# Optimization experiments

Measured on AMD Instinct MI355X. Metric: run time of the kernel, lower is better.

The kernel has to match this reference:

```python
import jax, jax.numpy as jnp
import numpy as np

N, E, D, T, R, H = 100000, 500000, 128, 3, 4, 8
DK = D // H
MAXLEN = 240
L = 2


def _rte_table():
    # Replicates RelTemporalEncoding sinusoidal table (note original precedence:
    # div_term = 1 / ((10000 ** arange(0, 2d, 2)) / d / 2); large exponents overflow
    # to inf in fp32 -> div entries become 0, matching torch behaviour).
    pos = jnp.arange(MAXLEN, dtype=jnp.float32)[:, None]            # [240, 1]
    ar = jnp.arange(0.0, 2 * D, 2.0, dtype=jnp.float32)             # [D]
    div = 1.0 / (jnp.power(jnp.float32(10000.0), ar) / D / 2.0)
    ang = pos * div                                                  # [240, D]
    s = np.float32(1.0 / np.sqrt(D))
    tab = jnp.zeros((MAXLEN, 2 * D), jnp.float32)
    tab = tab.at[:, 0::2].set(jnp.sin(ang) * s)
    tab = tab.at[:, 1::2].set(jnp.cos(ang) * s)
    return tab


def _typed_linear(x, W, b, types):
    # per-row type-specific affine: small fixed loop over node types
    out = jnp.zeros((x.shape[0], W.shape[-1]), x.dtype)
    for t in range(W.shape[0]):
        m = (types == t)[:, None].astype(x.dtype)
        out = out + m * (x @ W[t] + b[t])
    return out


def _typed_mm(x, W, types):
    out = jnp.zeros((x.shape[0], W.shape[-1]), x.dtype)
    for t in range(W.shape[0]):
        out = out + (types == t)[:, None].astype(x.dtype) * (x @ W[t])
    return out


def _hgt_layer(x, node_type, src, tgt, edge_type, edge_time, rte_tab,
               Wk, bk, Wq, bq, Wv, bv, Wa, ba, rel_pri, rel_att, rel_msg,
               skip, rte_w, rte_b):
    st = node_type[src]
    tt = node_type[tgt]
    # node-level typed projections (Q uses raw target feats; K/V bias+feat part)
    Qn = _typed_linear(x, Wq, bq, node_type)
    Kn = _typed_linear(x, Wk, bk, node_type)
    Vn = _typed_linear(x, Wv, bv, node_type)
    # per-edge temporal encoding added to source features before K/V linears;
    # linearity lets us add its typed projection (no double bias)
    rte = rte_tab[edge_time] @ rte_w + rte_b                         # [E, D]
    q = Qn[tgt].reshape(-1, H, DK)
    k = (Kn[src] + _typed_mm(rte, Wk, st)).reshape(-1, H, DK)
    v = (Vn[src] + _typed_mm(rte, Wv, st)).reshape(-1, H, DK)
    k2 = jnp.zeros_like(k)
    v2 = jnp.zeros_like(v)
    for r in range(R):  # small fixed relation loop, masked per-edge
        m = (edge_type == r)[:, None, None].astype(x.dtype)
        k2 = k2 + m * jnp.einsum('ehk,hkl->ehl', k, rel_att[r])
        v2 = v2 + m * jnp.einsum('ehk,hkl->ehl', v, rel_msg[r])
    pri = rel_pri[tt, edge_type, st]                                 # [E, H]
    score = (q * k2).sum(-1) * pri / np.float32(np.sqrt(DK))         # [E, H]
    # scatter-softmax over edges grouped by target node
    mx = jax.ops.segment_max(score, tgt, num_segments=N)
    ex = jnp.exp(score - mx[tgt])
    den = jax.ops.segment_sum(ex, tgt, num_segments=N)
    att = ex / den[tgt]
    msg = (v2 * att[:, :, None]).reshape(-1, D)
    aggr = jax.ops.segment_sum(msg, tgt, num_segments=N)             # [N, D]
    h = jax.nn.gelu(aggr, approximate=False)
    trans = _typed_linear(h, Wa, ba, node_type)
    alpha = jax.nn.sigmoid(skip)[node_type][:, None]
    return alpha * trans + (1.0 - alpha) * x


def setup_inputs() -> dict:
    key = jax.random.key(0)
    ks = jax.random.split(key, 20)
    s = np.float32(1.0 / np.sqrt(D))
    return {
        'node_feature': jax.random.normal(ks[0], (N, D), jnp.float32),
        'node_type': jax.random.randint(ks[1], (N,), 0, T, jnp.int32),
        'edge_index': jax.random.randint(ks[2], (2, E), 0, N, jnp.int32),
        'edge_type': jax.random.randint(ks[3], (E,), 0, R, jnp.int32),
        'edge_time': jax.random.randint(ks[4], (E,), 0, MAXLEN, jnp.int32),
        'adapt_w': jax.random.normal(ks[5], (T, D, D), jnp.float32) * s,
        'adapt_b': jax.random.normal(ks[6], (T, D), jnp.float32) * 0.01,
        'Wk': jax.random.normal(ks[7], (L, T, D, D), jnp.float32) * s,
        'bk': jax.random.normal(ks[8], (L, T, D), jnp.float32) * 0.01,
        'Wq': jax.random.normal(ks[9], (L, T, D, D), jnp.float32) * s,
        'bq': jax.random.normal(ks[10], (L, T, D), jnp.float32) * 0.01,
        'Wv': jax.random.normal(ks[11], (L, T, D, D), jnp.float32) * s,
        'bv': jax.random.normal(ks[12], (L, T, D), jnp.float32) * 0.01,
        'Wa': jax.random.normal(ks[13], (L, T, D, D), jnp.float32) * s,
        'ba': jax.random.normal(ks[14], (L, T, D), jnp.float32) * 0.01,
        'rel_pri': jnp.ones((L, T, R, T, H), jnp.float32),
        'rel_att': jax.random.normal(ks[15], (L, R, H, DK, DK), jnp.float32) * np.float32(1.0 / np.sqrt(DK)),
        'rel_msg': jax.random.normal(ks[16], (L, R, H, DK, DK), jnp.float32) * np.float32(1.0 / np.sqrt(DK)),
        'skip': jnp.ones((L, T), jnp.float32),
        'rte_w': jax.random.normal(ks[17], (L, 2 * D, D), jnp.float32) * np.float32(1.0 / np.sqrt(2 * D)),
        'rte_b': jax.random.normal(ks[18], (L, D), jnp.float32) * 0.01,
    }


def reference(node_feature, node_type, edge_index, edge_type, edge_time,
              adapt_w, adapt_b, Wk, bk, Wq, bq, Wv, bv, Wa, ba,
              rel_pri, rel_att, rel_msg, skip, rte_w, rte_b):
    rte_tab = _rte_table()
    src, tgt = edge_index[0], edge_index[1]
    # GNN input adaptation: typed linear + tanh (dropout = 0 / eval mode)
    x = jnp.tanh(_typed_linear(node_feature, adapt_w, adapt_b, node_type))
    for l in range(L):
        x = _hgt_layer(x, node_type, src, tgt, edge_type, edge_time, rte_tab,
                       Wk[l], bk[l], Wq[l], bq[l], Wv[l], bv[l], Wa[l], ba[l],
                       rel_pri[l], rel_att[l], rel_msg[l], skip[l],
                       rte_w[l], rte_b[l])
    return x
```

## Files before the change

kernel.cpp:

```cpp
#include <hip/hip_runtime.h>
#include <math.h>

#define NN 100000
#define EE 500000

__global__ void rte_tab_kernel(float* __restrict__ tab) {
    int p = blockIdx.x;
    int j = threadIdx.x;
    int m = j >> 1;
    float pf = (float)pow(10000.0, (double)(2 * m));
    float dv = 1.0f / (pf / 128.0f / 2.0f);
    float ang = (float)p * dv;
    const float s = 0.08838834764831845f;
    float v = (j & 1) ? (cosf(ang) * s) : (sinf(ang) * s);
    tab[p * 256 + j] = v;
}

__global__ void rte_proj_kernel(const float* __restrict__ tab,
                                const float* __restrict__ rte_w,
                                const float* __restrict__ rte_b,
                                float* __restrict__ proj) {
    __shared__ float row[256];
    int p = blockIdx.x;
    int c = threadIdx.x;
    for (int i = threadIdx.x; i < 256; i += 128) row[i] = tab[p * 256 + i];
    __syncthreads();
    float acc = rte_b[c];
    #pragma unroll 8
    for (int q = 0; q < 256; ++q) acc += row[q] * rte_w[q * 128 + c];
    proj[p * 128 + c] = acc;
}

__global__ void ktv_kernel(const float* __restrict__ proj,
                           const float* __restrict__ Wk,
                           const float* __restrict__ Wv,
                           float* __restrict__ ktv) {
    __shared__ float row[128];
    int b = blockIdx.x;
    int t = b / 240, p = b % 240;
    int c = threadIdx.x;
    row[c] = proj[p * 128 + c];
    __syncthreads();
    const float* wk = Wk + t * 16384 + c;
    const float* wv = Wv + t * 16384 + c;
    float ak = 0.f, av = 0.f;
    #pragma unroll 8
    for (int q = 0; q < 128; ++q) {
        float rv = row[q];
        ak += rv * wk[q * 128];
        av += rv * wv[q * 128];
    }
    ktv[(size_t)b * 256 + c] = ak;
    ktv[(size_t)b * 256 + 128 + c] = av;
}

__global__ void hist_kernel(const int* __restrict__ tgt, int* __restrict__ cnt) {
    int e = blockIdx.x * blockDim.x + threadIdx.x;
    if (e < EE) atomicAdd(&cnt[tgt[e]], 1);
}

__global__ void scan_kernel(const int* __restrict__ cnt, int* __restrict__ row_start) {
    __shared__ int sdata[1024];
    __shared__ int s_running;
    if (threadIdx.x == 0) s_running = 0;
    __syncthreads();
    for (int base = 0; base < NN; base += 1024) {
        int i = base + (int)threadIdx.x;
        int v = (i < NN) ? cnt[i] : 0;
        sdata[threadIdx.x] = v;
        __syncthreads();
        int acc = v;
        for (int off = 1; off < 1024; off <<= 1) {
            int t = (threadIdx.x >= (unsigned)off) ? sdata[threadIdx.x - off] : 0;
            __syncthreads();
            acc += t;
            sdata[threadIdx.x] = acc;
            __syncthreads();
        }
        int run = s_running;
        if (i < NN) row_start[i] = run + acc - v;
        __syncthreads();
        if (threadIdx.x == 1023) s_running = run + sdata[1023];
        __syncthreads();
    }
    if (threadIdx.x == 0) row_start[NN] = s_running;
}

__global__ void scatter_meta_kernel(const int* __restrict__ esrc,
                                    const int* __restrict__ etgt,
                                    const int* __restrict__ etype,
                                    const int* __restrict__ etime,
                                    const int* __restrict__ node_type,
                                    const int* __restrict__ row_start,
                                    int* __restrict__ fill,
                                    int4* __restrict__ meta) {
    int e = blockIdx.x * blockDim.x + threadIdx.x;
    if (e < EE) {
        int tgt = etgt[e];
        int src = esrc[e];
        int r = etype[e];
        int tm = etime[e];
        int st = node_type[src];
        int tt = node_type[tgt];
        int tb = st * 240 + tm;
        int pos = row_start[tgt] + atomicAdd(&fill[tgt], 1);
        meta[pos] = make_int4(src, (tb << 6) | (tt << 4) | (st << 2) | r, tgt, 0);
    }
}

__global__ void node_hist_kernel(const int* __restrict__ nt, int* __restrict__ tcnt) {
    __shared__ int lc[3];
    if (threadIdx.x < 3) lc[threadIdx.x] = 0;
    __syncthreads();
    int i = blockIdx.x * blockDim.x + threadIdx.x;
    if (i < NN) atomicAdd(&lc[nt[i]], 1);
    __syncthreads();
    if (threadIdx.x < 3) atomicAdd(&tcnt[threadIdx.x], lc[threadIdx.x]);
}

__global__ void node_scatter_kernel(const int* __restrict__ nt,
                                    const int* __restrict__ tcnt,
                                    int* __restrict__ fill3,
                                    int* __restrict__ order) {
    __shared__ int lc[3], lbase[3], lfill[3];
    if (threadIdx.x < 3) { lc[threadIdx.x] = 0; lfill[threadIdx.x] = 0; }
    __syncthreads();
    int i = blockIdx.x * blockDim.x + threadIdx.x;
    int t = -1;
    if (i < NN) { t = nt[i]; atomicAdd(&lc[t], 1); }
    __syncthreads();
    if (threadIdx.x < 3) lbase[threadIdx.x] = atomicAdd(&fill3[threadIdx.x], lc[threadIdx.x]);
    __syncthreads();
    if (i < NN) {
        int rank = atomicAdd(&lfill[t], 1);
        int tb = (t == 0) ? 0 : ((t == 1) ? tcnt[0] : tcnt[0] + tcnt[1]);
        order[tb + lbase[t] + rank] = i;
    }
}

template <int MODE>
__global__ __launch_bounds__(256) void typed_lin_kernel(
    const float* __restrict__ in, const int* __restrict__ nt,
    const int* __restrict__ order,
    const float* __restrict__ W, const float* __restrict__ b,
    const float* __restrict__ skip, float* __restrict__ out) {
    __shared__ float xs[32][128];
    __shared__ int rows[32];
    __shared__ int sty[32];
    int nb = blockIdx.x * 32;
    if (threadIdx.x < 32) {
        int r = order[nb + threadIdx.x];
        rows[threadIdx.x] = r;
        sty[threadIdx.x] = nt[r];
    }
    __syncthreads();
    for (int i = threadIdx.x; i < 1024; i += 256) {
        int nl = i >> 5, e4 = i & 31;
        *(float4*)&xs[nl][e4 * 4] = *(const float4*)(in + (size_t)rows[nl] * 128 + e4 * 4);
    }
    __syncthreads();
    int col = threadIdx.x & 127;
    int ng  = (threadIdx.x >> 7) * 16;
    int t0 = sty[ng];
    bool uni = true;
    #pragma unroll
    for (int ii = 1; ii < 16; ++ii) uni &= (sty[ng + ii] == t0);
    if (uni) {
        const float* w = W + t0 * 16384 + col;
        float bv = b[t0 * 128 + col];
        float alpha = (MODE == 1) ? (1.f / (1.f + __expf(-skip[t0]))) : 0.f;
        float acc[16];
        #pragma unroll
        for (int ii = 0; ii < 16; ++ii) acc[ii] = bv;
        for (int k0 = 0; k0 < 128; k0 += 4) {
            float w0 = w[(k0 + 0) * 128];
            float w1 = w[(k0 + 1) * 128];
            float w2 = w[(k0 + 2) * 128];
            float w3 = w[(k0 + 3) * 128];
            #pragma unroll
            for (int ii = 0; ii < 16; ++ii) {
                float4 xv = *(const float4*)&xs[ng + ii][k0];
                acc[ii] += xv.x * w0 + xv.y * w1 + xv.z * w2 + xv.w * w3;
            }
        }
        #pragma unroll
        for (int ii = 0; ii < 16; ++ii) {
            size_t gi = (size_t)rows[ng + ii] * 128 + col;
            if (MODE == 0) out[gi] = tanhf(acc[ii]);
            else           out[gi] = alpha * acc[ii] + (1.f - alpha) * out[gi];
        }
    } else {
        for (int ii = 0; ii < 16; ++ii) {
            int nl = ng + ii;
            int t = sty[nl];
            const float* w = W + t * 16384 + col;
            float acc = b[t * 128 + col];
            #pragma unroll 8
            for (int k = 0; k < 128; ++k) acc += xs[nl][k] * w[k * 128];
            size_t gi = (size_t)rows[nl] * 128 + col;
            if (MODE == 0) out[gi] = tanhf(acc);
            else {
                float alpha = 1.f / (1.f + __expf(-skip[t]));
                out[gi] = alpha * acc + (1.f - alpha) * out[gi];
            }
        }
    }
}

__global__ __launch_bounds__(256) void qkv_kernel(
    const float* __restrict__ x, const int* __restrict__ nt,
    const int* __restrict__ order,
    const float* __restrict__ Wq, const float* __restrict__ bq,
    const float* __restrict__ Wk, const float* __restrict__ bk,
    const float* __restrict__ Wv, const float* __restrict__ bv,
    float* __restrict__ Qn, float* __restrict__ KV) {
    __shared__ float xs[32][128];
    __shared__ int rows[32];
    __shared__ int sty[32];
    int nb = blockIdx.x * 32;
    if (threadIdx.x < 32) {
        int r = order[nb + threadIdx.x];
        rows[threadIdx.x] = r;
        sty[threadIdx.x] = nt[r];
    }
    __syncthreads();
    for (int i = threadIdx.x; i < 1024; i += 256) {
        int nl = i >> 5, e4 = i & 31;
        *(float4*)&xs[nl][e4 * 4] = *(const float4*)(x + (size_t)rows[nl] * 128 + e4 * 4);
    }
    __syncthreads();
    int col = threadIdx.x & 127;
    int ng  = (threadIdx.x >> 7) * 16;
    int t0 = sty[ng];
    bool uni = true;
    #pragma unroll
    for (int ii = 1; ii < 16; ++ii) uni &= (sty[ng + ii] == t0);
    if (uni) {
        const float* wq = Wq + t0 * 16384 + col;
        const float* wk = Wk + t0 * 16384 + col;
        const float* wv = Wv + t0 * 16384 + col;
        float bqv = bq[t0 * 128 + col];
        float bkv = bk[t0 * 128 + col];
        float bvv = bv[t0 * 128 + col];
        float aq[16], ak[16], av[16];
        #pragma unroll
        for (int ii = 0; ii < 16; ++ii) { aq[ii] = bqv; ak[ii] = bkv; av[ii] = bvv; }
        for (int k0 = 0; k0 < 128; k0 += 4) {
            float q0 = wq[(k0 + 0) * 128], q1 = wq[(k0 + 1) * 128];
            float q2 = wq[(k0 + 2) * 128], q3 = wq[(k0 + 3) * 128];
            float k0w = wk[(k0 + 0) * 128], k1w = wk[(k0 + 1) * 128];
            float k2w = wk[(k0 + 2) * 128], k3w = wk[(k0 + 3) * 128];
            float v0 = wv[(k0 + 0) * 128], v1 = wv[(k0 + 1) * 128];
            float v2 = wv[(k0 + 2) * 128], v3 = wv[(k0 + 3) * 128];
            #pragma unroll
            for (int ii = 0; ii < 16; ++ii) {
                float4 xv = *(const float4*)&xs[ng + ii][k0];
                aq[ii] += xv.x * q0 + xv.y * q1 + xv.z * q2 + xv.w * q3;
                ak[ii] += xv.x * k0w + xv.y * k1w + xv.z * k2w + xv.w * k3w;
                av[ii] += xv.x * v0 + xv.y * v1 + xv.z * v2 + xv.w * v3;
            }
        }
        #pragma unroll
        for (int ii = 0; ii < 16; ++ii) {
            size_t row = (size_t)rows[ng + ii];
            Qn[row * 128 + col] = aq[ii];
            KV[row * 256 + col] = ak[ii];
            KV[row * 256 + 128 + col] = av[ii];
        }
    } else {
        for (int ii = 0; ii < 16; ++ii) {
            int nl = ng + ii;
            int t = sty[nl];
            const float* wq = Wq + t * 16384 + col;
            const float* wk = Wk + t * 16384 + col;
            const float* wv = Wv + t * 16384 + col;
            float aq = bq[t * 128 + col];
            float ak = bk[t * 128 + col];
            float av = bv[t * 128 + col];
            #pragma unroll 4
            for (int k = 0; k < 128; ++k) {
                float xv = xs[nl][k];
                aq += xv * wq[k * 128];
                ak += xv * wk[k * 128];
                av += xv * wv[k * 128];
            }
            size_t row = (size_t)rows[nl];
            Qn[row * 128 + col] = aq;
            KV[row * 256 + col] = ak;
            KV[row * 256 + 128 + col] = av;
        }
    }
}

__global__ __launch_bounds__(256) void edge_kernel(
    const float* __restrict__ Qn, const float* __restrict__ KV,
    const float* __restrict__ ktv, const int4* __restrict__ meta,
    const int* __restrict__ node_type,
    const float* __restrict__ rel_pri, const float* __restrict__ rel_att,
    const float* __restrict__ rel_msg, const int* __restrict__ row_start,
    float* __restrict__ h_out) {
    __shared__ float smem[4][1056];
    __shared__ int chs[4];
    int w = threadIdx.x >> 6;
    int lane = threadIdx.x & 63;
    int n = blockIdx.x * 4 + w;
    float* qAs_w   = smem[w];
    float* scratch = smem[w] + 512;

    int e_beg = row_start[n], e_end = row_start[n + 1];
    int tt = node_type[n];
    int4 mm0 = make_int4(0, 0, 0, 0);
    if (e_beg + lane < e_end) mm0 = meta[e_beg + lane];

    float2 q2 = *(const float2*)(Qn + (size_t)n * 128 + lane * 2);
    *(float2*)&scratch[lane * 2] = q2;
    if (lane == 0) chs[w] = (e_end - e_beg + 63) >> 6;
    __syncthreads();
    int nch = max(max(chs[0], chs[1]), max(chs[2], chs[3]));

    #pragma unroll
    for (int u = 0; u < 8; ++u) {
        int f = u * 64 + lane;
        int rem = f & 127;
        int hh = rem >> 4;
        const float4* A4 = (const float4*)(rel_att + (size_t)f * 16);
        float4 a0 = A4[0], a1 = A4[1], a2 = A4[2], a3 = A4[3];
        const float* qq = &scratch[hh * 16];
        float val = a0.x * qq[0] + a0.y * qq[1] + a0.z * qq[2] + a0.w * qq[3]
                  + a1.x * qq[4] + a1.y * qq[5] + a1.z * qq[6] + a1.w * qq[7]
                  + a2.x * qq[8] + a2.y * qq[9] + a2.z * qq[10] + a2.w * qq[11]
                  + a3.x * qq[12] + a3.y * qq[13] + a3.z * qq[14] + a3.w * qq[15];
        qAs_w[f] = val;
    }
    __syncthreads();

    int j = lane >> 3, h = lane & 7;
    int h2 = lane >> 3, d0 = lane * 2;
    int cp = d0 & 15;
    float ls = 0.f;
    float2 a0v = {0.f, 0.f}, a1v = {0.f, 0.f}, a2v = {0.f, 0.f}, a3v = {0.f, 0.f};
    int rmask = 0;

    for (int c = 0; c < nch; ++c) {
        int cb = e_beg + (c << 6);
        bool active = cb < e_end;
        int4 mm = mm0;
        if (c > 0) {
            mm = make_int4(0, 0, 0, 0);
            if (active && (cb + lane) < e_end) mm = meta[cb + lane];
        }
        if (active) {
            int nss = (min(64, e_end - cb) + 7) >> 3;
            for (int ss = 0; ss < nss; ++ss) {
                int icb = ss << 3;
                int ei = cb + icb + j;
                bool valid = ei < e_end;
                int mxs = __shfl(mm.x, icb + j, 64);
                int mys = __shfl(mm.y, icb + j, 64);
                int r = mys & 3, st = (mys >> 2) & 3, tb = mys >> 6;
                const float4* kp = (const float4*)(KV + (size_t)mxs * 256 + h * 16);
                const float4* tp = (const float4*)(ktv + (size_t)tb * 256 + h * 16);
                float4 k0 = kp[0], k1 = kp[1], k2 = kp[2], k3 = kp[3];
                float4 t0 = tp[0], t1 = tp[1], t2 = tp[2], t3 = tp[3];
                const float* qa = qAs_w + r * 128 + h * 16;
                float s = (k0.x + t0.x) * qa[0]  + (k0.y + t0.y) * qa[1]
                        + (k0.z + t0.z) * qa[2]  + (k0.w + t0.w) * qa[3]
                        + (k1.x + t1.x) * qa[4]  + (k1.y + t1.y) * qa[5]
                        + (k1.z + t1.z) * qa[6]  + (k1.w + t1.w) * qa[7]
                        + (k2.x + t2.x) * qa[8]  + (k2.y + t2.y) * qa[9]
                        + (k2.z + t2.z) * qa[10] + (k2.w + t2.w) * qa[11]
                        + (k3.x + t3.x) * qa[12] + (k3.y + t3.y) * qa[13]
                        + (k3.z + t3.z) * qa[14] + (k3.w + t3.w) * qa[15];
                float pri = rel_pri[((tt * 4 + r) * 3 + st) * 8 + h];
                float p = valid ? __expf(s * pri * 0.25f) : 0.f;
                scratch[icb * 8 + lane] = p;
                ls += p;
            }
        }
        __syncthreads();
        if (active) {
            int cdeg = min(64, e_end - cb);
            int mx = mm.x, my = mm.y;
            #pragma unroll 4
            for (int i = 0; i < cdeg; ++i) {
                int src  = __shfl(mx, i, 64);
                int code = __shfl(my, i, 64);
                int r = code & 3;
                float pv = scratch[i * 8 + h2];
                float2 v1 = *(const float2*)(KV + (size_t)src * 256 + 128 + d0);
                float2 v2 = *(const float2*)(ktv + (size_t)(code >> 6) * 256 + 128 + d0);
                float vx = pv * (v1.x + v2.x);
                float vy = pv * (v1.y + v2.y);
                rmask |= (1 << r);
                switch (r) {
                    case 0: a0v.x += vx; a0v.y += vy; break;
                    case 1: a1v.x += vx; a1v.y += vy; break;
                    case 2: a2v.x += vx; a2v.y += vy; break;
                    default: a3v.x += vx; a3v.y += vy; break;
                }
            }
        }
        __syncthreads();
    }

    ls += __shfl_xor(ls, 8, 64);
    ls += __shfl_xor(ls, 16, 64);
    ls += __shfl_xor(ls, 32, 64);

    int li = h2 * 17 + cp;
    scratch[0 * 136 + li] = a0v.x; scratch[0 * 136 + li + 1] = a0v.y;
    scratch[1 * 136 + li] = a1v.x; scratch[1 * 136 + li + 1] = a1v.y;
    scratch[2 * 136 + li] = a2v.x; scratch[2 * 136 + li + 1] = a2v.y;
    scratch[3 * 136 + li] = a3v.x; scratch[3 * 136 + li + 1] = a3v.y;
    __syncthreads();
    float o0 = 0.f, o1 = 0.f;
    const float* M = rel_msg + h2 * 256 + cp;
    #pragma unroll
    for (int r = 0; r < 4; ++r) {
        if (rmask & (1 << r)) {
            #pragma unroll
            for (int i = 0; i < 16; ++i) {
                float av = scratch[r * 136 + h2 * 17 + i];
                float2 mm2 = *(const float2*)(M + r * 2048 + i * 16);
                o0 += av * mm2.x;
                o1 += av * mm2.y;
            }
        }
    }
    float lst = __shfl(ls, h2, 64);
    float iv = (lst > 0.f) ? (1.f / lst) : 0.f;
    o0 *= iv; o1 *= iv;
    o0 = 0.5f * o0 * (1.f + erff(o0 * 0.7071067811865475f));
    o1 = 0.5f * o1 * (1.f + erff(o1 * 0.7071067811865475f));
    *(float2*)(h_out + (size_t)n * 128 + d0) = make_float2(o0, o1);
}

extern "C" void kernel_launch(void* const* d_in, const int* in_sizes, int n_in,
                              void* d_out, int out_size, void* d_ws, size_t ws_size,
                              hipStream_t stream) {
    const float* node_feature = (const float*)d_in[0];
    const int*   node_type    = (const int*)d_in[1];
    const int*   edge_index   = (const int*)d_in[2];
    const int*   edge_type    = (const int*)d_in[3];
    const int*   edge_time    = (const int*)d_in[4];
    const float* adapt_w      = (const float*)d_in[5];
    const float* adapt_b      = (const float*)d_in[6];
    const float* Wk           = (const float*)d_in[7];
    const float* bk           = (const float*)d_in[8];
    const float* Wq           = (const float*)d_in[9];
    const float* bq           = (const float*)d_in[10];
    const float* Wv           = (const float*)d_in[11];
    const float* bv           = (const float*)d_in[12];
    const float* Wa           = (const float*)d_in[13];
    const float* ba           = (const float*)d_in[14];
    const float* rel_pri      = (const float*)d_in[15];
    const float* rel_att      = (const float*)d_in[16];
    const float* rel_msg      = (const float*)d_in[17];
    const float* skip         = (const float*)d_in[18];
    const float* rte_w        = (const float*)d_in[19];
    const float* rte_b        = (const float*)d_in[20];
    float* out = (float*)d_out;

    const size_t ND = (size_t)NN * 128;
    float* Qn     = (float*)d_ws;
    float* KV     = Qn + ND;
    float* rtab   = KV + 2 * ND;
    float* rproj  = rtab + 240 * 256;
    float* ktv    = rproj + 240 * 128;
    int*   cnt    = (int*)(ktv + 720 * 256);
    int*   fill   = cnt + NN;
    int*   row_st = fill + NN;
    int*   order  = row_st + NN + 4;
    int*   tcnt   = order + NN;
    int*   fill3  = tcnt + 4;
    int4*  meta   = (int4*)(fill3 + 4);

    const int* esrc = edge_index;
    const int* etgt = edge_index + EE;

    hipMemsetAsync(cnt, 0, 2 * NN * sizeof(int), stream);
    hipMemsetAsync(tcnt, 0, 8 * sizeof(int), stream);
    rte_tab_kernel<<<240, 256, 0, stream>>>(rtab);
    hist_kernel<<<(EE + 255) / 256, 256, 0, stream>>>(etgt, cnt);
    scan_kernel<<<1, 1024, 0, stream>>>(cnt, row_st);
    scatter_meta_kernel<<<(EE + 255) / 256, 256, 0, stream>>>(esrc, etgt, edge_type,
                                                              edge_time, node_type,
                                                              row_st, fill, meta);
    node_hist_kernel<<<(NN + 255) / 256, 256, 0, stream>>>(node_type, tcnt);
    node_scatter_kernel<<<(NN + 255) / 256, 256, 0, stream>>>(node_type, tcnt, fill3, order);

    typed_lin_kernel<0><<<NN / 32, 256, 0, stream>>>(node_feature, node_type, order,
                                                     adapt_w, adapt_b, nullptr, out);

    for (int l = 0; l < 2; ++l) {
        const float* Wk_l = Wk + l * 49152;  const float* bk_l = bk + l * 384;
        const float* Wq_l = Wq + l * 49152;  const float* bq_l = bq + l * 384;
        const float* Wv_l = Wv + l * 49152;  const float* bv_l = bv + l * 384;
        const float* Wa_l = Wa + l * 49152;  const float* ba_l = ba + l * 384;
        const float* pri_l = rel_pri + l * 288;
        const float* att_l = rel_att + l * 8192;
        const float* msg_l = rel_msg + l * 8192;
        const float* skip_l = skip + l * 3;
        const float* rte_w_l = rte_w + l * 32768;
        const float* rte_b_l = rte_b + l * 128;

        rte_proj_kernel<<<240, 128, 0, stream>>>(rtab, rte_w_l, rte_b_l, rproj);
        ktv_kernel<<<720, 128, 0, stream>>>(rproj, Wk_l, Wv_l, ktv);
        qkv_kernel<<<NN / 32, 256, 0, stream>>>(out, node_type, order, Wq_l, bq_l,
                                                Wk_l, bk_l, Wv_l, bv_l, Qn, KV);
        edge_kernel<<<NN / 4, 256, 0, stream>>>(Qn, KV, ktv, meta, node_type,
                                                pri_l, att_l, msg_l, row_st,
                                                Qn );
        typed_lin_kernel<1><<<NN / 32, 256, 0, stream>>>(Qn, node_type, order, Wa_l, ba_l,
                                                         skip_l, out);
    }
}
```

Before: 1.873 ms.

## Stage relation matrices in LDS and process eight nodes per wave in edge kernel

New measurement: 1.680 ms. -10.3%, faster.

```diff
diff --git a/kernel.cpp b/kernel.cpp
--- a/kernel.cpp
+++ b/kernel.cpp
@@ -299,70 +299,85 @@
     const float* __restrict__ rel_pri, const float* __restrict__ rel_att,
     const float* __restrict__ rel_msg, const int* __restrict__ row_start,
     float* __restrict__ h_out) {
-    __shared__ float smem[4][1056];
-    __shared__ int chs[4];
-    int w = threadIdx.x >> 6;
-    int lane = threadIdx.x & 63;
-    int n = blockIdx.x * 4 + w;
-    float* qAs_w   = smem[w];
-    float* scratch = smem[w] + 512;
-
-    int e_beg = row_start[n], e_end = row_start[n + 1];
-    int tt = node_type[n];
-    int4 mm0 = make_int4(0, 0, 0, 0);
-    if (e_beg + lane < e_end) mm0 = meta[e_beg + lane];
-
-    float2 q2 = *(const float2*)(Qn + (size_t)n * 128 + lane * 2);
-    *(float2*)&scratch[lane * 2] = q2;
-    if (lane == 0) chs[w] = (e_end - e_beg + 63) >> 6;
-    __syncthreads();
-    int nch = max(max(chs[0], chs[1]), max(chs[2], chs[3]));
-
-    #pragma unroll
-    for (int u = 0; u < 8; ++u) {
-        int f = u * 64 + lane;
-        int rem = f & 127;
-        int hh = rem >> 4;
-        const float4* A4 = (const float4*)(rel_att + (size_t)f * 16);
-        float4 a0 = A4[0], a1 = A4[1], a2 = A4[2], a3 = A4[3];
-        const float* qq = &scratch[hh * 16];
-        float val = a0.x * qq[0] + a0.y * qq[1] + a0.z * qq[2] + a0.w * qq[3]
-                  + a1.x * qq[4] + a1.y * qq[5] + a1.z * qq[6] + a1.w * qq[7]
-                  + a2.x * qq[8] + a2.y * qq[9] + a2.z * qq[10] + a2.w * qq[11]
-                  + a3.x * qq[12] + a3.y * qq[13] + a3.z * qq[14] + a3.w * qq[15];
-        qAs_w[f] = val;
-    }
-    __syncthreads();
-
-    int j = lane >> 3, h = lane & 7;
+    __shared__ float At[16 * 512];
+    __shared__ float Ml[4 * 2080];
+    __shared__ float scr[4][768];
+
+    int tid = threadIdx.x;
+    for (int g0 = tid * 4; g0 < 8192; g0 += 1024) {
+        float4 a = *(const float4*)(rel_att + g0);
+        int la = g0 & 15, ka = (g0 >> 4) & 15, rh = g0 >> 8;
+        At[(la + 0) * 512 + rh * 16 + ka] = a.x;
+        At[(la + 1) * 512 + rh * 16 + ka] = a.y;
+        At[(la + 2) * 512 + rh * 16 + ka] = a.z;
+        At[(la + 3) * 512 + rh * 16 + ka] = a.w;
+        float4 m = *(const float4*)(rel_msg + g0);
+        int cm = g0 & 15, im = (g0 >> 4) & 15, hm = (g0 >> 8) & 7, rm = g0 >> 11;
+        *(float4*)&Ml[rm * 2080 + hm * 260 + im * 16 + cm] = m;
+    }
+    __syncthreads();
+
+    int w = tid >> 6;
+    int lane = tid & 63;
+    float* qA = scr[w];
+    float* pl = scr[w] + 512;
+
+    int hE = lane >> 4;
+    int j  = lane >> 3, h = lane & 7;
     int h2 = lane >> 3, d0 = lane * 2;
-    int cp = d0 & 15;
-    float ls = 0.f;
-    float2 a0v = {0.f, 0.f}, a1v = {0.f, 0.f}, a2v = {0.f, 0.f}, a3v = {0.f, 0.f};
-    int rmask = 0;
-
-    for (int c = 0; c < nch; ++c) {
-        int cb = e_beg + (c << 6);
-        bool active = cb < e_end;
-        int4 mm = mm0;
-        if (c > 0) {
-            mm = make_int4(0, 0, 0, 0);
-            if (active && (cb + lane) < e_end) mm = meta[cb + lane];
-        }
-        if (active) {
-            int nss = (min(64, e_end - cb) + 7) >> 3;
+    int cp = (lane & 7) * 2;
+
+    for (int g = 0; g < 8; ++g) {
+        int n = blockIdx.x * 32 + w * 8 + g;
+        int e_beg = row_start[n], e_end = row_start[n + 1];
+        int tt = node_type[n];
+
+        const float4* qp  = (const float4*)(Qn + (size_t)n * 128 + hE * 16);
+        const float4* qp2 = (const float4*)(Qn + (size_t)n * 128 + 64 + hE * 16);
+        float4 qE0 = qp[0],  qE1 = qp[1],  qE2 = qp[2],  qE3 = qp[3];
+        float4 qO0 = qp2[0], qO1 = qp2[1], qO2 = qp2[2], qO3 = qp2[3];
+
+        int4 mm = make_int4(0, 0, 0, 0);
+        if (lane < 32 && e_beg + lane < e_end) mm = meta[e_beg + lane];
+
+        #pragma unroll
+        for (int u = 0; u < 8; ++u) {
+            int f = u * 64 + lane;
+            const float* a = &At[f];
+            float4 qa0 = (u & 1) ? qO0 : qE0;
+            float4 qa1 = (u & 1) ? qO1 : qE1;
+            float4 qa2 = (u & 1) ? qO2 : qE2;
+            float4 qa3 = (u & 1) ? qO3 : qE3;
+            float val = a[0*512]*qa0.x + a[1*512]*qa0.y + a[2*512]*qa0.z + a[3*512]*qa0.w
+                      + a[4*512]*qa1.x + a[5*512]*qa1.y + a[6*512]*qa1.z + a[7*512]*qa1.w
+                      + a[8*512]*qa2.x + a[9*512]*qa2.y + a[10*512]*qa2.z + a[11*512]*qa2.w
+                      + a[12*512]*qa3.x + a[13*512]*qa3.y + a[14*512]*qa3.z + a[15*512]*qa3.w;
+            qA[f] = val;
+        }
+
+        float ls = 0.f;
+        float2 a0v = {0.f,0.f}, a1v = {0.f,0.f}, a2v = {0.f,0.f}, a3v = {0.f,0.f};
+        int rmask = 0;
+
+        for (int cb = e_beg; cb < e_end; cb += 32) {
+            if (cb > e_beg) {
+                mm = make_int4(0, 0, 0, 0);
+                if (lane < 32 && cb + lane < e_end) mm = meta[cb + lane];
+            }
+            int cdeg = min(32, e_end - cb);
+            int nss = (cdeg + 7) >> 3;
             for (int ss = 0; ss < nss; ++ss) {
-                int icb = ss << 3;
-                int ei = cb + icb + j;
+                int sl = ss * 8 + j;
+                int ei = cb + sl;
                 bool valid = ei < e_end;
-                int mxs = __shfl(mm.x, icb + j, 64);
-                int mys = __shfl(mm.y, icb + j, 64);
+                int mxs = __shfl(mm.x, sl, 64);
+                int mys = __shfl(mm.y, sl, 64);
                 int r = mys & 3, st = (mys >> 2) & 3, tb = mys >> 6;
                 const float4* kp = (const float4*)(KV + (size_t)mxs * 256 + h * 16);
                 const float4* tp = (const float4*)(ktv + (size_t)tb * 256 + h * 16);
                 float4 k0 = kp[0], k1 = kp[1], k2 = kp[2], k3 = kp[3];
                 float4 t0 = tp[0], t1 = tp[1], t2 = tp[2], t3 = tp[3];
-                const float* qa = qAs_w + r * 128 + h * 16;
+                const float* qa = qA + r * 128 + h * 16;
                 float s = (k0.x + t0.x) * qa[0]  + (k0.y + t0.y) * qa[1]
                         + (k0.z + t0.z) * qa[2]  + (k0.w + t0.w) * qa[3]
                         + (k1.x + t1.x) * qa[4]  + (k1.y + t1.y) * qa[5]
@@ -373,20 +388,16 @@
                         + (k3.z + t3.z) * qa[14] + (k3.w + t3.w) * qa[15];
                 float pri = rel_pri[((tt * 4 + r) * 3 + st) * 8 + h];
                 float p = valid ? __expf(s * pri * 0.25f) : 0.f;
-                scratch[icb * 8 + lane] = p;
+                pl[ss * 64 + lane] = p;
                 ls += p;
             }
-        }
-        __syncthreads();
-        if (active) {
-            int cdeg = min(64, e_end - cb);
             int mx = mm.x, my = mm.y;
             #pragma unroll 4
             for (int i = 0; i < cdeg; ++i) {
                 int src  = __shfl(mx, i, 64);
                 int code = __shfl(my, i, 64);
                 int r = code & 3;
-                float pv = scratch[i * 8 + h2];
+                float pv = pl[i * 8 + h2];
                 float2 v1 = *(const float2*)(KV + (size_t)src * 256 + 128 + d0);
                 float2 v2 = *(const float2*)(ktv + (size_t)(code >> 6) * 256 + 128 + d0);
                 float vx = pv * (v1.x + v2.x);
@@ -400,39 +411,37 @@
                 }
             }
         }
-        __syncthreads();
-    }
-
-    ls += __shfl_xor(ls, 8, 64);
-    ls += __shfl_xor(ls, 16, 64);
-    ls += __shfl_xor(ls, 32, 64);
-
-    int li = h2 * 17 + cp;
-    scratch[0 * 136 + li] = a0v.x; scratch[0 * 136 + li + 1] = a0v.y;
-    scratch[1 * 136 + li] = a1v.x; scratch[1 * 136 + li + 1] = a1v.y;
-    scratch[2 * 136 + li] = a2v.x; scratch[2 * 136 + li + 1] = a2v.y;
-    scratch[3 * 136 + li] = a3v.x; scratch[3 * 136 + li + 1] = a3v.y;
-    __syncthreads();
-    float o0 = 0.f, o1 = 0.f;
-    const float* M = rel_msg + h2 * 256 + cp;
-    #pragma unroll
-    for (int r = 0; r < 4; ++r) {
-        if (rmask & (1 << r)) {
-            #pragma unroll
-            for (int i = 0; i < 16; ++i) {
-                float av = scratch[r * 136 + h2 * 17 + i];
-                float2 mm2 = *(const float2*)(M + r * 2048 + i * 16);
-                o0 += av * mm2.x;
-                o1 += av * mm2.y;
-            }
-        }
-    }
-    float lst = __shfl(ls, h2, 64);
-    float iv = (lst > 0.f) ? (1.f / lst) : 0.f;
-    o0 *= iv; o1 *= iv;
-    o0 = 0.5f * o0 * (1.f + erff(o0 * 0.7071067811865475f));
-    o1 = 0.5f * o1 * (1.f + erff(o1 * 0.7071067811865475f));
-    *(float2*)(h_out + (size_t)n * 128 + d0) = make_float2(o0, o1);
+
+        ls += __shfl_xor(ls, 8, 64);
+        ls += __shfl_xor(ls, 16, 64);
+        ls += __shfl_xor(ls, 32, 64);
+        float lst = __shfl(ls, h2, 64);
+        float iv = (lst > 0.f) ? (1.f / lst) : 0.f;
+
+        float o0 = 0.f, o1 = 0.f;
+        const float* Mb = &Ml[h2 * 260 + cp];
+        #pragma unroll
+        for (int r = 0; r < 4; ++r) {
+            if (rmask & (1 << r)) {
+                float sx, sy;
+                #pragma unroll
+                for (int m = 0; m < 8; ++m) {
+                    if (r == 0)      { sx = __shfl(a0v.x, h2 * 8 + m, 64); sy = __shfl(a0v.y, h2 * 8 + m, 64); }
+                    else if (r == 1) { sx = __shfl(a1v.x, h2 * 8 + m, 64); sy = __shfl(a1v.y, h2 * 8 + m, 64); }
+                    else if (r == 2) { sx = __shfl(a2v.x, h2 * 8 + m, 64); sy = __shfl(a2v.y, h2 * 8 + m, 64); }
+                    else             { sx = __shfl(a3v.x, h2 * 8 + m, 64); sy = __shfl(a3v.y, h2 * 8 + m, 64); }
+                    float2 m0 = *(const float2*)&Mb[r * 2080 + (2 * m) * 16];
+                    float2 m1 = *(const float2*)&Mb[r * 2080 + (2 * m + 1) * 16];
+                    o0 += sx * m0.x + sy * m1.x;
+                    o1 += sx * m0.y + sy * m1.y;
+                }
+            }
+        }
+        o0 *= iv; o1 *= iv;
+        o0 = 0.5f * o0 * (1.f + erff(o0 * 0.7071067811865475f));
+        o1 = 0.5f * o1 * (1.f + erff(o1 * 0.7071067811865475f));
+        *(float2*)(h_out + (size_t)n * 128 + d0) = make_float2(o0, o1);
+    }
 }
 
 extern "C" void kernel_launch(void* const* d_in, const int* in_sizes, int n_in,
@@ -508,9 +517,9 @@
         ktv_kernel<<<720, 128, 0, stream>>>(rproj, Wk_l, Wv_l, ktv);
         qkv_kernel<<<NN / 32, 256, 0, stream>>>(out, node_type, order, Wq_l, bq_l,
                                                 Wk_l, bk_l, Wv_l, bv_l, Qn, KV);
-        edge_kernel<<<NN / 4, 256, 0, stream>>>(Qn, KV, ktv, meta, node_type,
-                                                pri_l, att_l, msg_l, row_st,
-                                                Qn );
+        edge_kernel<<<NN / 32, 256, 0, stream>>>(Qn, KV, ktv, meta, node_type,
+                                                 pri_l, att_l, msg_l, row_st,
+                                                 Qn );
         typed_lin_kernel<1><<<NN / 32, 256, 0, stream>>>(Qn, node_type, order, Wa_l, ba_l,
                                                          skip_l, out);
     }
```
